# Optimization experiments

Hardware: AMD Instinct MI355X
Metric: run time of the kernel (lower is better)

Reference implementation:

```python
import jax, jax.numpy as jnp
import numpy as np

V, E, H, D, A, P = 8000, 384, 512, 512, 512, 128
B, N = 16, 128
NEG = -1.0e9


def _lstm(x, Wih, Whh, b, reverse=False):
    # x: (B, T, E); torch gate order i, f, g, o
    Hd = Whh.shape[1]
    def step(carry, xt):
        h, c = carry
        gates = xt @ Wih.T + h @ Whh.T + b
        i, f, g, o = jnp.split(gates, 4, axis=-1)
        c = jax.nn.sigmoid(f) * c + jax.nn.sigmoid(i) * jnp.tanh(g)
        h = jax.nn.sigmoid(o) * jnp.tanh(c)
        return (h, c), h
    xs = jnp.swapaxes(x, 0, 1)
    if reverse:
        xs = xs[::-1]
    init = (jnp.zeros((x.shape[0], Hd), x.dtype), jnp.zeros((x.shape[0], Hd), x.dtype))
    _, hs = jax.lax.scan(step, init, xs)
    if reverse:
        hs = hs[::-1]
    return jnp.swapaxes(hs, 0, 1)


def _forward(src_ids, src_mask, confusionset_mask, emb, Wih_f, Whh_f, b_f, Wih_b, Whh_b, b_b,
             Wih_d, Whh_d, b_d, W1, W2, v_att, combine_W, combine_b, vocab_W, vocab_b,
             Wg_W, Wg_b, ptr_W, ptr_b, ps_W, ps_b):
    x = emb[src_ids]                                                     # (B,N,E)
    # bidirectional encoder
    enc_hs = jnp.concatenate([_lstm(x, Wih_f, Whh_f, b_f),
                              _lstm(x, Wih_b, Whh_b, b_b, reverse=True)], axis=-1)  # (B,N,2H)
    # decoder LSTMCell unrolled over max_len=N steps (teacher forcing on src chars)
    dec_h = _lstm(x, Wih_d, Whh_d, b_d)                                  # (B,N,D)
    # Bahdanau additive attention
    dterm = dec_h @ W1.T                                                 # (B,N,A)
    eterm = enc_hs @ W2.T                                                # (B,N,A)
    score = jnp.tanh(dterm[:, :, None, :] + eterm[:, None, :, :]) @ v_att  # (B,T,n)
    score = jnp.where(src_mask[:, None, :] == 0, NEG, score)
    alpha = jax.nn.softmax(score, axis=-1)
    context = jnp.einsum('btn,bnh->bth', alpha, enc_hs)                  # (B,T,2H)
    combined = jnp.tanh(jnp.concatenate([dec_h, context], axis=-1) @ combine_W.T + combine_b)  # (B,T,D)
    vocab_logits = combined @ vocab_W.T + vocab_b                        # (B,T,V)
    vocab_logits = jnp.where(confusionset_mask == 0, NEG, vocab_logits)
    # pointer logits: Locj = (t == j) indicator as extra feature
    loc = jnp.eye(N, dtype=combined.dtype)                               # (T,n)
    base = combined @ ptr_W[:, :D].T + ptr_b                             # (B,T,P)
    ph = jnp.tanh(base[:, :, None, :] + loc[None, :, :, None] * ptr_W[:, D][None, None, None, :])  # (B,T,n,P)
    pos_scores = ph @ ps_W + ps_b                                        # (B,T,n)
    sentinel = jnp.tanh(combined @ Wg_W.T + Wg_b).sum(-1, keepdims=True) # (B,T,1)
    pointer_logits = jnp.concatenate([pos_scores, sentinel], axis=-1)    # (B,T,n+1)
    pad_mask = jnp.concatenate([src_mask, jnp.ones((src_mask.shape[0], 1), src_mask.dtype)], axis=1)
    pointer_logits = jnp.where(pad_mask[:, None, :] == 0, NEG, pointer_logits)
    return pointer_logits, vocab_logits


def setup_inputs():
    ks = iter(jax.random.split(jax.random.key(0), 40))
    def g(shape, s=0.05):
        return jax.random.normal(next(ks), shape, jnp.float32) * s
    inp = {
        'src_ids': jax.random.randint(next(ks), (B, N), 1, V),
        'src_mask': jnp.ones((B, N), jnp.int32),
        'confusionset_mask': jax.random.randint(next(ks), (B, N, V), 0, 2).astype(jnp.int32),
        'emb': g((V, E)).at[0].set(0.0),  # padding_idx=0 row zeroed
        'Wih_f': g((4 * H, E)), 'Whh_f': g((4 * H, H)), 'b_f': g((4 * H,)),
        'Wih_b': g((4 * H, E)), 'Whh_b': g((4 * H, H)), 'b_b': g((4 * H,)),
        'Wih_d': g((4 * D, E)), 'Whh_d': g((4 * D, D)), 'b_d': g((4 * D,)),
        'W1': g((A, D)), 'W2': g((A, 2 * H)), 'v_att': g((A,)),
        'combine_W': g((D, D + 2 * H)), 'combine_b': g((D,)),
        'vocab_W': g((V, D)), 'vocab_b': g((V,)),
        'Wg_W': g((D, D)), 'Wg_b': g((D,)),
        'ptr_W': g((P, D + 1)), 'ptr_b': g((P,)),
        'ps_W': g((P,)), 'ps_b': g(()),
    }
    return inp


def reference(src_ids, src_mask, confusionset_mask, emb, Wih_f, Whh_f, b_f, Wih_b, Whh_b, b_b,
              Wih_d, Whh_d, b_d, W1, W2, v_att, combine_W, combine_b, vocab_W, vocab_b,
              Wg_W, Wg_b, ptr_W, ptr_b, ps_W, ps_b):
    return _forward(src_ids, src_mask, confusionset_mask, emb, Wih_f, Whh_f, b_f, Wih_b, Whh_b, b_b,
                    Wih_d, Whh_d, b_d, W1, W2, v_att, combine_W, combine_b, vocab_W, vocab_b,
                    Wg_W, Wg_b, ptr_W, ptr_b, ps_W, ps_b)
```

## Files before the change

### kernel.cpp

```cpp
#include <hip/hip_runtime.h>
#include <hip/hip_bf16.h>
#include <math.h>

#define NEGV -1000000000.0f

static constexpr int B_ = 16, N_ = 128, BN_ = 2048;
static constexpr int E_ = 384, V_ = 8000;

typedef __attribute__((ext_vector_type(8))) short short8v;
typedef __attribute__((ext_vector_type(4))) float f32x4;

__device__ inline float wave_sum(float v) {
#pragma unroll
  for (int o = 32; o; o >>= 1) v += __shfl_xor(v, o);
  return v;
}
__device__ inline float wave_max(float v) {
#pragma unroll
  for (int o = 32; o; o >>= 1) v = fmaxf(v, __shfl_xor(v, o));
  return v;
}
__device__ inline float fast_tanh(float x) {
  return 1.f - 2.f / (1.f + __expf(2.f * x));
}
__device__ inline float fast_tanh_pre(float x2) {
  return 1.f - 2.f / (1.f + __expf(x2));
}
__device__ inline float fast_sig(float x) {
  return 1.f / (1.f + __expf(-x));
}
__device__ __forceinline__ void gl16(const void* g, void* l) {
  __builtin_amdgcn_global_load_lds((const __attribute__((address_space(1))) void*)g,
                                   (__attribute__((address_space(3))) void*)l, 16, 0, 0);
}

struct CastArgs {
  const float* s[6];
  unsigned long long d[6];
  int base[6];
  int total;
  int special;
};
__device__ inline void cast_body(const CastArgs& a, int gsize, int gid0) {
  const int nq = a.total >> 2;
  for (int q = gid0; q < nq; q += gsize) {
    const int e = q << 2;
    int k = 5;
    while (e < a.base[k]) --k;
    const int i = e - a.base[k];
    __hip_bfloat16* dst = (__hip_bfloat16*)a.d[k] + i;
    if (k == a.special) {
      const int row = i >> 9, col = i & 511;
      const float* sp = a.s[k] + (size_t)row * 513 + col;
#pragma unroll
      for (int u = 0; u < 4; ++u) dst[u] = __float2bfloat16(sp[u]);
    } else {
      float4 v = *(const float4*)(a.s[k] + i);
      __hip_bfloat16 h0 = __float2bfloat16(v.x), h1 = __float2bfloat16(v.y);
      __hip_bfloat16 h2 = __float2bfloat16(v.z), h3 = __float2bfloat16(v.w);
      ushort4 u4 = {*(unsigned short*)&h0, *(unsigned short*)&h1,
                    *(unsigned short*)&h2, *(unsigned short*)&h3};
      *(ushort4*)dst = u4;
    }
  }
}

__global__ __launch_bounds__(256) void prologue_kernel(
    const int* __restrict__ ids, const float* __restrict__ emb,
    __hip_bfloat16* __restrict__ xb, __hip_bfloat16* __restrict__ hbuf,
    CastArgs c1) {
  const int bid = blockIdx.x, tid = threadIdx.x;
  if (bid < 256) {
    for (int row = bid; row < 2048; row += 256) {
      const int id = ids[row];
      for (int e = tid; e < E_; e += 256)
        xb[(size_t)row * E_ + e] = __float2bfloat16(emb[(size_t)id * E_ + e]);
    }
  } else if (bid < 288) {
    const unsigned total = 3u * 128u * 8192u * 2u;
    const float pf = __builtin_bit_cast(float, 0x7f7f7f7fu);
    f32x4 pat = {pf, pf, pf, pf};
    char* base = (char*)hbuf;
    for (unsigned off = (unsigned)((bid - 256) * 256 + tid) * 16u; off < total;
         off += 32u * 256u * 16u) {
      asm volatile("global_store_dwordx4 %0, %1, %2 sc0 sc1"
                   :: "v"(off), "v"(pat), "s"(base) : "memory");
    }
  } else {
    cast_body(c1, 256 * 256, (bid - 288) * 256 + tid);
  }
}

template <int ACT, bool MASK>
__device__ __forceinline__ void gemm128_impl(
    const __hip_bfloat16* A, int lda, const __hip_bfloat16* W, int ldw,
    const float* bias, float* C, int ldc, __hip_bfloat16* Cb, int ldcb,
    int N, int K, const int* mask, int ldm, int m0, int n0,
    __hip_bfloat16 (*Al)[4096], __hip_bfloat16 (*Bl)[4096]) {
  const int tid = threadIdx.x;
  const int wid = tid >> 6, lane = tid & 63;
  const int nkt = K >> 5;
  const int rm = (wid >> 1) << 6, rn = (wid & 1) << 6;
  const int lrow = lane & 15, kq = lane >> 4;
  const int fs = ((lrow >> 1) & 3) << 4;

  f32x4 acc[4][4];
#pragma unroll
  for (int i = 0; i < 4; ++i)
#pragma unroll
    for (int j = 0; j < 4; ++j) acc[i][j] = {0.f, 0.f, 0.f, 0.f};

  auto stage = [&](int bi, int kt) {
#pragma unroll
    for (int c = 0; c < 2; ++c) {
      const int p = ((c * 4 + wid) << 6) + lane;
      const int row = p >> 2, cb = (p & 3) << 4;
      const int sw = ((row >> 1) & 3) << 4;
      const unsigned loff = (unsigned)__builtin_amdgcn_readfirstlane((c * 4 + wid) << 10);
      {
        const char* src = (const char*)A + ((size_t)(m0 + row) * lda + (size_t)kt * 32) * 2 + (cb ^ sw);
        gl16(src, (char*)&Al[bi][0] + loff);
      }
      {
        int gr = n0 + row;
        if (gr >= N) gr = N - 1;
        const char* src = (const char*)W + ((size_t)gr * ldw + (size_t)kt * 32) * 2 + (cb ^ sw);
        gl16(src, (char*)&Bl[bi][0] + loff);
      }
    }
  };
  auto compute = [&](int bi) {
    const char* Ab = (const char*)&Al[bi][0];
    const char* Bb = (const char*)&Bl[bi][0];
    const int roff = (kq << 4) ^ fs;
    short8v a[4], b[4];
#pragma unroll
    for (int i = 0; i < 4; ++i)
      a[i] = *(const short8v*)(Ab + (rm + i * 16 + lrow) * 64 + roff);
#pragma unroll
    for (int j = 0; j < 4; ++j)
      b[j] = *(const short8v*)(Bb + (rn + j * 16 + lrow) * 64 + roff);
#pragma unroll
    for (int i = 0; i < 4; ++i)
#pragma unroll
      for (int j = 0; j < 4; ++j)
        acc[i][j] = __builtin_amdgcn_mfma_f32_16x16x32_bf16(a[i], b[j], acc[i][j], 0, 0, 0);
  };

  stage(0, 0);
  for (int kt = 0; kt < nkt; ++kt) {
    __syncthreads();
    if (kt + 1 < nkt) stage((kt + 1) & 1, kt + 1);
    compute(kt & 1);
  }

#pragma unroll
  for (int i = 0; i < 4; ++i) {
#pragma unroll
    for (int r = 0; r < 4; ++r) {
      const int m = m0 + rm + i * 16 + kq * 4 + r;
#pragma unroll
      for (int j = 0; j < 4; ++j) {
        const int n = n0 + rn + j * 16 + lrow;
        if (n < N) {
          float v = acc[i][j][r] + (bias ? bias[n] : 0.f);
          if (ACT == 1) v = fast_tanh(v);
          if (MASK) {
            if (mask[(size_t)m * ldm + n] == 0) v = NEGV;
          }
          if (C) C[(size_t)m * ldc + n] = v;
          if (Cb) Cb[(size_t)m * ldcb + n] = __float2bfloat16(v);
        }
      }
    }
  }
}

__device__ __forceinline__ void gemm64_impl(
    const __hip_bfloat16* A, int lda, const __hip_bfloat16* W, int ldw,
    const float* bias, const float* bias2,
    float* C, int ldc, float* C2, __hip_bfloat16* Cb, int ldcb,
    int K, int act, int trout, int m0, int n0, char* AlB, char* BlB) {
  const int tid = threadIdx.x;
  const int wid = tid >> 6, lane = tid & 63;
  const int nkt = K >> 5;
  const int rm = (wid >> 1) << 5, rn = (wid & 1) << 5;
  const int lrow = lane & 15, kq = lane >> 4;
  const int fs = ((lrow >> 1) & 3) << 4;

  f32x4 acc[2][2];
#pragma unroll
  for (int i = 0; i < 2; ++i)
#pragma unroll
    for (int j = 0; j < 2; ++j) acc[i][j] = {0.f, 0.f, 0.f, 0.f};

  auto stage = [&](int bi, int kt) {
    const int row = tid >> 2, cb = (tid & 3) << 4;
    const int sw = ((row >> 1) & 3) << 4;
    const unsigned loff = (unsigned)__builtin_amdgcn_readfirstlane(wid << 10);
    {
      const char* src = (const char*)A + ((size_t)(m0 + row) * lda + (size_t)kt * 32) * 2 + (cb ^ sw);
      gl16(src, AlB + bi * 4096 + loff);
    }
    {
      const char* src = (const char*)W + ((size_t)(n0 + row) * ldw + (size_t)kt * 32) * 2 + (cb ^ sw);
      gl16(src, BlB + bi * 4096 + loff);
    }
  };
  auto compute = [&](int bi) {
    const char* Ab = AlB + bi * 4096;
    const char* Bb = BlB + bi * 4096;
    const int roff = (kq << 4) ^ fs;
    short8v a[2], b[2];
#pragma unroll
    for (int i = 0; i < 2; ++i)
      a[i] = *(const short8v*)(Ab + (rm + i * 16 + lrow) * 64 + roff);
#pragma unroll
    for (int j = 0; j < 2; ++j)
      b[j] = *(const short8v*)(Bb + (rn + j * 16 + lrow) * 64 + roff);
#pragma unroll
    for (int i = 0; i < 2; ++i)
#pragma unroll
      for (int j = 0; j < 2; ++j)
        acc[i][j] = __builtin_amdgcn_mfma_f32_16x16x32_bf16(a[i], b[j], acc[i][j], 0, 0, 0);
  };

  stage(0, 0);
  for (int kt = 0; kt < nkt; ++kt) {
    __syncthreads();
    if (kt + 1 < nkt) stage((kt + 1) & 1, kt + 1);
    compute(kt & 1);
  }

#pragma unroll
  for (int i = 0; i < 2; ++i) {
#pragma unroll
    for (int r = 0; r < 4; ++r) {
      const int m = m0 + rm + i * 16 + kq * 4 + r;
#pragma unroll
      for (int j = 0; j < 2; ++j) {
        const int n = n0 + rn + j * 16 + lrow;
        float v = acc[i][j][r];
        if (trout == 2) {
          if (n < 512) {
            C[(size_t)m * ldc + n] = fast_tanh(v + bias[n]);
          } else {
            C2[(size_t)m * 128 + (n - 512)] = v + bias2[n - 512];
          }
        } else {
          if (act == 2) v *= 2.f;
          else {
            v += (bias ? bias[n] : 0.f);
            if (act == 1) v = fast_tanh(v);
          }
          if (trout == 1) {
            Cb[(((size_t)(m >> 7) * 512 + n) << 7) + (m & 127)] = __float2bfloat16(v);
          } else {
            if (C) C[(size_t)m * ldc + n] = v;
            if (Cb) Cb[(size_t)m * ldcb + n] = __float2bfloat16(v);
          }
        }
      }
    }
  }
}

__global__ __launch_bounds__(256) void xproj_kernel(
    const __hip_bfloat16* __restrict__ A, const __hip_bfloat16* __restrict__ Wih,
    const float* __restrict__ b0, const float* __restrict__ b1,
    const float* __restrict__ b2, __hip_bfloat16* __restrict__ xproj16) {
  __shared__ __hip_bfloat16 Al[2][4096], Bl[2][4096];
  const int z = blockIdx.z;
  const float* bias = (z == 0) ? b0 : (z == 1 ? b1 : b2);
  gemm128_impl<0, false>(A, E_, Wih + (size_t)z * 2048 * 384, E_, bias,
                         nullptr, 0, xproj16 + (size_t)z * BN_ * 2048, 2048,
                         2048, E_, nullptr, 0, blockIdx.y * 128,
                         blockIdx.x * 128, Al, Bl);
}

__global__ __launch_bounds__(256) void qk_kernel(
    const __hip_bfloat16* __restrict__ catb, const __hip_bfloat16* __restrict__ ehsb,
    const __hip_bfloat16* __restrict__ w1, const __hip_bfloat16* __restrict__ w2,
    float* __restrict__ dterm, __hip_bfloat16* __restrict__ etT) {
  __shared__ char AlB[8192], BlB[8192];
  const int bid = blockIdx.x;
  if (bid < 256) {
    const int bx = bid & 7, by = bid >> 3;
    gemm64_impl(catb, 1536, w1, 512, nullptr, nullptr, dterm, 512, nullptr,
                nullptr, 0, 512, 2, 0, by * 64, bx * 64, AlB, BlB);
  } else {
    const int l = bid - 256;
    const int bx = l & 7, by = l >> 3;
    gemm64_impl(ehsb, 1024, w2, 1024, nullptr, nullptr, nullptr, 0, nullptr,
                etT, 0, 1024, 2, 1, by * 64, bx * 64, AlB, BlB);
  }
}

__global__ __launch_bounds__(256) void ctx_kernel(
    const __hip_bfloat16* __restrict__ alphab, const __hip_bfloat16* __restrict__ ehsT,
    __hip_bfloat16* __restrict__ catbCtx) {
  __shared__ char AlB[8192], BlB[8192];
  const int z = blockIdx.z;
  gemm64_impl(alphab + (size_t)z * 128 * 128, 128,
              ehsT + (size_t)z * 1024 * 128, 128, nullptr, nullptr, nullptr, 0,
              nullptr, catbCtx + (size_t)z * 128 * 1536, 1536, 128, 0, 0,
              blockIdx.y * 64, blockIdx.x * 64, AlB, BlB);
}

__global__ __launch_bounds__(256) void comb_kernel(
    const __hip_bfloat16* __restrict__ catb, const __hip_bfloat16* __restrict__ combw,
    const float* __restrict__ comb_b, __hip_bfloat16* __restrict__ combb) {
  __shared__ char AlB[8192], BlB[8192];
  gemm64_impl(catb, 1536, combw, 1536, comb_b, nullptr, nullptr, 0, nullptr,
              combb, 512, 1536, 1, 0, blockIdx.y * 64, blockIdx.x * 64, AlB, BlB);
}

__global__ __launch_bounds__(256) void tail_kernel(
    const __hip_bfloat16* __restrict__ combb, const __hip_bfloat16* __restrict__ vocw,
    const float* __restrict__ vocab_b, float* __restrict__ out1,
    const int* __restrict__ cmask,
    const __hip_bfloat16* __restrict__ wgw, const float* __restrict__ Wg_b,
    const float* __restrict__ ptr_b, float* __restrict__ wgout,
    float* __restrict__ baseb) {
  __shared__ __hip_bfloat16 Al[2][4096], Bl[2][4096];
  const int bid = blockIdx.x;
  if (bid < 1008) {
    const int bx = bid % 63, by = bid / 63;
    gemm128_impl<0, true>(combb, 512, vocw, 512, vocab_b, out1, V_, nullptr, 0,
                          V_, 512, cmask, V_, by * 128, bx * 128, Al, Bl);
  } else {
    const int l = bid - 1008;
    const int bx = l % 10, by = l / 10;
    gemm64_impl(combb, 512, wgw, 512, Wg_b, ptr_b, wgout, 512, baseb, nullptr,
                0, 512, 0, 2, by * 64, bx * 64, (char*)Al, (char*)Bl);
  }
}

__global__ __launch_bounds__(256) void fused_kernel(
    const __hip_bfloat16* __restrict__ xp16,
    const float* __restrict__ whhF, const float* __restrict__ whhB,
    const float* __restrict__ whhD,
    __hip_bfloat16* __restrict__ hbuf,
    __hip_bfloat16* __restrict__ ehsb, __hip_bfloat16* __restrict__ ehsT,
    __hip_bfloat16* __restrict__ catb,
    CastArgs ca2) {
  extern __shared__ char sm[];
  const int bid = blockIdx.x;
  const int tid = threadIdx.x;

  if (bid >= 96) {
    cast_body(ca2, 64 * 256, (bid - 96) * 256 + tid);
    return;
  }

  const int l = bid >> 5, g = bid & 31;
  const int lane = tid & 63, wid = tid >> 6;
  char* smW = sm;
  char* smH = sm + 65536;
  __hip_bfloat16* hout = (__hip_bfloat16*)(sm + 65536 + 16384);
  char* hist = sm + 65536 + 16384 + 512;

  const float* wsrc = (l == 0) ? whhF : ((l == 1) ? whhB : whhD);
  auto cv = [](float x) -> unsigned {
    __hip_bfloat16 h = __float2bfloat16(x);
    return (unsigned)*(unsigned short*)&h;
  };
  for (int p = tid; p < 4096; p += 256) {
    const int r = p >> 6, cb = (p & 63) << 4;
    const int grow = (r & 3) * 512 + (g << 4) + (r >> 2);
    const float* srcp = wsrc + (size_t)grow * 512 + ((p & 63) << 3);
    float4 u0 = *(const float4*)srcp;
    float4 u1 = *(const float4*)(srcp + 4);
    uint4 q;
    q.x = cv(u0.x) | (cv(u0.y) << 16);
    q.y = cv(u0.z) | (cv(u0.w) << 16);
    q.z = cv(u1.x) | (cv(u1.y) << 16);
    q.w = cv(u1.z) | (cv(u1.w) << 16);
    *(uint4*)(smW + r * 1024 + (cb ^ ((r & 7) << 4))) = q;
  }

  const int lrow = lane & 15, kq = lane >> 4;
  const int swz = (lrow & 7) << 4;
  const char* aB = smW + (wid * 16 + lrow) * 1024;
  const char* bB = smH + lrow * 1024;
  const int dl16 = wid * 4 + kq;
  const int dg = (g << 4) + dl16;
  const int bb = lrow;
  const bool rev = (l == 1);
  const __hip_bfloat16* xl = xp16 + (size_t)l * 2048 * 2048;
  __hip_bfloat16* hb_l = hbuf + (size_t)l * 128 * 8192;
  const int gq = tid >> 3;
  const int b0 = (tid & 7) * 2;
  const int gb = gq * 32;
  const int sw0 = (b0 & 7) << 4, sw1 = ((b0 + 1) & 7) << 4;
  float c = 0.f;

  for (int s = 0; s < 128; ++s) {
    const int t = rev ? 127 - s : s;
    const size_t xro = (size_t)(bb * 128 + t) * 2048 + dg;
    const float xgi = __bfloat162float(xl[xro]);
    const float xgf = __bfloat162float(xl[xro + 512]);
    const float xgg = __bfloat162float(xl[xro + 1024]);
    const float xgo = __bfloat162float(xl[xro + 1536]);

    if (s > 0) {
      if (gq != g) {
        const char* hsrc = (const char*)(hb_l + (size_t)(s - 1) * 8192);
        const unsigned loff = (unsigned)(tid * 64);
        unsigned hv;
        while (true) {
          asm volatile(
              "global_load_ushort %0, %1, %2 sc0 sc1\n\t"
              "s_waitcnt vmcnt(0)"
              : "=&v"(hv) : "v"(loff), "s"(hsrc) : "memory");
          if ((hv & 0xffffu) != 0x7f7fu) break;
          __builtin_amdgcn_s_sleep(1);
        }
        f32x4 q0, q1, q2, q3;
        asm volatile(
            "global_load_dwordx4 %0, %4, %5 sc0 sc1\n\t"
            "global_load_dwordx4 %1, %4, %5 offset:16 sc0 sc1\n\t"
            "global_load_dwordx4 %2, %4, %5 offset:32 sc0 sc1\n\t"
            "global_load_dwordx4 %3, %4, %5 offset:48 sc0 sc1\n\t"
            "s_waitcnt vmcnt(0)"
            : "=&v"(q0), "=&v"(q1), "=&v"(q2), "=&v"(q3)
            : "v"(loff), "s"(hsrc) : "memory");
        *(f32x4*)(smH + b0 * 1024 + (gb ^ sw0)) = q0;
        *(f32x4*)(smH + b0 * 1024 + ((gb + 16) ^ sw0)) = q1;
        *(f32x4*)(smH + (b0 + 1) * 1024 + (gb ^ sw1)) = q2;
        *(f32x4*)(smH + (b0 + 1) * 1024 + ((gb + 16) ^ sw1)) = q3;
      } else {
        const char* hl = (const char*)hout + b0 * 32;
        f32x4 c0 = *(const f32x4*)(hl);
        f32x4 c1 = *(const f32x4*)(hl + 16);
        f32x4 c2 = *(const f32x4*)(hl + 32);
        f32x4 c3 = *(const f32x4*)(hl + 48);
        *(f32x4*)(smH + b0 * 1024 + (gb ^ sw0)) = c0;
        *(f32x4*)(smH + b0 * 1024 + ((gb + 16) ^ sw0)) = c1;
        *(f32x4*)(smH + (b0 + 1) * 1024 + (gb ^ sw1)) = c2;
        *(f32x4*)(smH + (b0 + 1) * 1024 + ((gb + 16) ^ sw1)) = c3;
      }
    } else {
      const f32x4 z = {0.f, 0.f, 0.f, 0.f};
      *(f32x4*)(smH + b0 * 1024 + (gb ^ sw0)) = z;
      *(f32x4*)(smH + b0 * 1024 + ((gb + 16) ^ sw0)) = z;
      *(f32x4*)(smH + (b0 + 1) * 1024 + (gb ^ sw1)) = z;
      *(f32x4*)(smH + (b0 + 1) * 1024 + ((gb + 16) ^ sw1)) = z;
    }
    __syncthreads();

    f32x4 acc0 = {0.f, 0.f, 0.f, 0.f}, acc1 = {0.f, 0.f, 0.f, 0.f};
#pragma unroll
    for (int kt = 0; kt < 16; kt += 2) {
      const int off0 = ((kt * 64 + (kq << 4)) ^ swz);
      const int off1 = (((kt + 1) * 64 + (kq << 4)) ^ swz);
      short8v a0 = *(const short8v*)(aB + off0);
      short8v b0v = *(const short8v*)(bB + off0);
      short8v a1 = *(const short8v*)(aB + off1);
      short8v b1v = *(const short8v*)(bB + off1);
      acc0 = __builtin_amdgcn_mfma_f32_16x16x32_bf16(a0, b0v, acc0, 0, 0, 0);
      acc1 = __builtin_amdgcn_mfma_f32_16x16x32_bf16(a1, b1v, acc1, 0, 0, 0);
    }
    const f32x4 acc = acc0 + acc1;

    const float gi = acc[0] + xgi;
    const float gf = acc[1] + xgf;
    const float gg = acc[2] + xgg;
    const float go = acc[3] + xgo;
    c = fmaf(fast_sig(gf), c, fast_sig(gi) * fast_tanh(gg));
    const float h = fast_sig(go) * fast_tanh(c);
    __hip_bfloat16 hb16 = __float2bfloat16(h);
    const unsigned short hraw = *(unsigned short*)&hb16;
    hout[bb * 16 + dl16] = hb16;
    *(unsigned short*)(hist + s * 512 + (bb * 16 + dl16) * 2) = hraw;
    __syncthreads();

    if (s < 127 && wid == (s & 3) && (lane < 32)) {
      f32x4 hv4 = *(const f32x4*)((const char*)hout + lane * 16);
      char* hdst = (char*)(hb_l + (size_t)s * 8192);
      asm volatile("global_store_dwordx4 %0, %1, %2 sc0 sc1"
                   :: "v"((unsigned)((g << 9) + lane * 16)), "v"(hv4), "s"(hdst)
                   : "memory");
    }
  }

  __syncthreads();
  const int bb2 = tid >> 4, lo2 = tid & 15;
  if (l < 2) {
    const int hoff = (bb2 * 16 + lo2) * 2;
    char* dstT = (char*)(ehsT + ((size_t)bb2 * 1024 + l * 512 + (g << 4) + lo2) * 128);
    for (int tc = 0; tc < 128; tc += 32) {
      unsigned v[16];
#pragma unroll
      for (int w = 0; w < 16; ++w) {
        const int t0 = tc + 2 * w;
        const int s0 = rev ? 127 - t0 : t0;
        const int s1 = rev ? 126 - t0 : t0 + 1;
        unsigned a = *(const unsigned short*)(hist + s0 * 512 + hoff);
        unsigned b2 = *(const unsigned short*)(hist + s1 * 512 + hoff);
        v[w] = a | (b2 << 16);
      }
#pragma unroll
      for (int q = 0; q < 4; ++q)
        *(uint4*)(dstT + tc * 2 + q * 16) =
            make_uint4(v[q * 4], v[q * 4 + 1], v[q * 4 + 2], v[q * 4 + 3]);
    }
    for (int k = 0; k < 8; ++k) {
      const int t = lo2 * 8 + k;
      const int s0 = rev ? 127 - t : t;
      const char* srcp = hist + s0 * 512 + bb2 * 32;
      uint4 ra = *(const uint4*)srcp;
      uint4 rb = *(const uint4*)(srcp + 16);
      char* dp = (char*)(ehsb + ((size_t)(bb2 * 128 + t)) * 1024 + l * 512 + (g << 4));
      *(uint4*)dp = ra;
      *(uint4*)(dp + 16) = rb;
    }
  } else {
    for (int k = 0; k < 8; ++k) {
      const int t = lo2 * 8 + k;
      const char* srcp = hist + t * 512 + bb2 * 32;
      uint4 ra = *(const uint4*)srcp;
      uint4 rb = *(const uint4*)(srcp + 16);
      char* dp = (char*)(catb + ((size_t)(bb2 * 128 + t)) * 1536 + (g << 4));
      *(uint4*)dp = ra;
      *(uint4*)(dp + 16) = rb;
    }
  }
}

__global__ __launch_bounds__(256) void score_kernel(
    const float* __restrict__ dterm, const __hip_bfloat16* __restrict__ etT,
    const float* __restrict__ v_att, const int* __restrict__ src_mask,
    __hip_bfloat16* __restrict__ alphab) {
  const int b = blockIdx.x >> 5, tg = blockIdx.x & 31;
  const int t0 = tg * 4;
  const int tid = threadIdx.x;
  __shared__ float dt[4][512], vs[512], red[4][4][128], al[4][128];
  for (int i = tid; i < 2048; i += 256)
    dt[i >> 9][i & 511] = dterm[((size_t)(b * 128 + t0 + (i >> 9))) * 512 + (i & 511)];
  vs[tid] = v_att[tid];
  vs[tid + 256] = v_att[256 + tid];
  __syncthreads();
  const int n0 = (tid & 63) << 1, ah = tid >> 6;
  {
    const __hip_bfloat16* ep = etT + (((size_t)b * 512 + ah * 128) << 7) + n0;
    const float* vp = vs + ah * 128;
    const float* dp0 = &dt[0][ah * 128];
    const float* dp1 = &dt[1][ah * 128];
    const float* dp2 = &dt[2][ah * 128];
    const float* dp3 = &dt[3][ah * 128];
    float p00 = 0, p01 = 0, p10 = 0, p11 = 0, p20 = 0, p21 = 0, p30 = 0, p31 = 0;
    for (int a = 0; a < 128; ++a) {
      const unsigned u = *(const unsigned*)(ep + ((size_t)a << 7));
      unsigned u0 = u << 16, u1 = u & 0xffff0000u;
      const float e0 = __builtin_bit_cast(float, u0);
      const float e1 = __builtin_bit_cast(float, u1);
      const float va = vp[a];
      p00 = fmaf(va, fast_tanh_pre(dp0[a] + e0), p00);
      p01 = fmaf(va, fast_tanh_pre(dp0[a] + e1), p01);
      p10 = fmaf(va, fast_tanh_pre(dp1[a] + e0), p10);
      p11 = fmaf(va, fast_tanh_pre(dp1[a] + e1), p11);
      p20 = fmaf(va, fast_tanh_pre(dp2[a] + e0), p20);
      p21 = fmaf(va, fast_tanh_pre(dp2[a] + e1), p21);
      p30 = fmaf(va, fast_tanh_pre(dp3[a] + e0), p30);
      p31 = fmaf(va, fast_tanh_pre(dp3[a] + e1), p31);
    }
    red[0][ah][n0] = p00; red[0][ah][n0 + 1] = p01;
    red[1][ah][n0] = p10; red[1][ah][n0 + 1] = p11;
    red[2][ah][n0] = p20; red[2][ah][n0 + 1] = p21;
    red[3][ah][n0] = p30; red[3][ah][n0 + 1] = p31;
  }
  __syncthreads();
#pragma unroll
  for (int tp = 0; tp < 2; ++tp) {
    const int tt = tp * 2 + (tid >> 7);
    const int n = tid & 127;
    float sc = red[tt][0][n] + red[tt][1][n] + red[tt][2][n] + red[tt][3][n];
    if (src_mask[b * 128 + n] == 0) sc = NEGV;
    al[tt][n] = sc;
  }
  __syncthreads();
  {
    const int tt = tid >> 6, lane = tid & 63;
    const float v0 = al[tt][lane], v1 = al[tt][lane + 64];
    const float m = wave_max(fmaxf(v0, v1));
    const float e0 = __expf(v0 - m), e1 = __expf(v1 - m);
    const float inv = 1.f / wave_sum(e0 + e1);
    __hip_bfloat16* ap = alphab + ((size_t)(b * 128 + t0 + tt)) * 128;
    ap[lane] = __float2bfloat16(e0 * inv);
    ap[lane + 64] = __float2bfloat16(e1 * inv);
  }
}

__global__ __launch_bounds__(256) void pointer_kernel(
    const float* __restrict__ base, const float* __restrict__ wgout,
    const float* __restrict__ ptr_W, const float* __restrict__ ps_W,
    const float* __restrict__ ps_b, const int* __restrict__ src_mask,
    float* __restrict__ out0) {
  const int bt = blockIdx.x;
  const int b = bt >> 7, t = bt & 127;
  const int tid = threadIdx.x;
  __shared__ float r0[4], r1[4], r2[4], fin[3];
  float off_p = 0.f, diag_p = 0.f, sent_p;
  if (tid < 128) {
    const float ba = base[(size_t)bt * 128 + tid];
    const float pw = ps_W[tid];
    off_p = tanhf(ba) * pw;
    diag_p = tanhf(ba + ptr_W[tid * 513 + 512]) * pw;
  }
  sent_p = wgout[(size_t)bt * 512 + tid] + wgout[(size_t)bt * 512 + 256 + tid];
  off_p = wave_sum(off_p);
  diag_p = wave_sum(diag_p);
  sent_p = wave_sum(sent_p);
  const int wid = tid >> 6, lane = tid & 63;
  if (lane == 0) { r0[wid] = off_p; r1[wid] = diag_p; r2[wid] = sent_p; }
  __syncthreads();
  if (tid == 0) {
    const float psb = ps_b[0];
    fin[0] = r0[0] + r0[1] + r0[2] + r0[3] + psb;
    fin[1] = r1[0] + r1[1] + r1[2] + r1[3] + psb;
    fin[2] = r2[0] + r2[1] + r2[2] + r2[3];
  }
  __syncthreads();
  const float s_off = fin[0], s_diag = fin[1], sent = fin[2];
  if (tid < 129) {
    float v;
    if (tid == 128) v = sent;
    else {
      v = (tid == t) ? s_diag : s_off;
      if (src_mask[b * 128 + tid] == 0) v = NEGV;
    }
    out0[(size_t)bt * 129 + tid] = v;
  }
}

extern "C" void kernel_launch(void* const* d_in, const int* in_sizes, int n_in,
                              void* d_out, int out_size, void* d_ws, size_t ws_size,
                              hipStream_t stream) {
  const int* src_ids   = (const int*)d_in[0];
  const int* src_mask  = (const int*)d_in[1];
  const int* cmask     = (const int*)d_in[2];
  const float* emb     = (const float*)d_in[3];
  const float* Wih_f   = (const float*)d_in[4];
  const float* Whh_f   = (const float*)d_in[5];
  const float* b_f     = (const float*)d_in[6];
  const float* Wih_b   = (const float*)d_in[7];
  const float* Whh_b   = (const float*)d_in[8];
  const float* b_b     = (const float*)d_in[9];
  const float* Wih_d   = (const float*)d_in[10];
  const float* Whh_d   = (const float*)d_in[11];
  const float* b_d     = (const float*)d_in[12];
  const float* W1      = (const float*)d_in[13];
  const float* W2      = (const float*)d_in[14];
  const float* v_att   = (const float*)d_in[15];
  const float* comb_W  = (const float*)d_in[16];
  const float* comb_b  = (const float*)d_in[17];
  const float* vocab_W = (const float*)d_in[18];
  const float* vocab_b = (const float*)d_in[19];
  const float* Wg_W    = (const float*)d_in[20];
  const float* Wg_b    = (const float*)d_in[21];
  const float* ptr_W   = (const float*)d_in[22];
  const float* ptr_b   = (const float*)d_in[23];
  const float* ps_W    = (const float*)d_in[24];
  const float* ps_b    = (const float*)d_in[25];
  (void)in_sizes; (void)n_in; (void)out_size; (void)ws_size;

  char* wsb = (char*)d_ws;
  size_t o = 0;
  auto alloc = [&](size_t bytes) { char* p = wsb + o; o = (o + bytes + 255) & ~(size_t)255; return p; };
  __hip_bfloat16* xb      = (__hip_bfloat16*)alloc((size_t)BN_ * E_ * 2);
  __hip_bfloat16* xproj16 = (__hip_bfloat16*)alloc((size_t)3 * BN_ * 2048 * 2);
  __hip_bfloat16* ehsb    = (__hip_bfloat16*)alloc((size_t)BN_ * 1024 * 2);
  __hip_bfloat16* ehsT    = (__hip_bfloat16*)alloc((size_t)16 * 1024 * 128 * 2);
  __hip_bfloat16* catb    = (__hip_bfloat16*)alloc((size_t)BN_ * 1536 * 2);
  float* dterm            = (float*)alloc((size_t)BN_ * 512 * 4);
  __hip_bfloat16* etT     = (__hip_bfloat16*)alloc((size_t)16 * 512 * 128 * 2);
  __hip_bfloat16* alphab  = (__hip_bfloat16*)alloc((size_t)BN_ * 128 * 2);
  __hip_bfloat16* combb   = (__hip_bfloat16*)alloc((size_t)BN_ * 512 * 2);
  float* wgout            = (float*)alloc((size_t)BN_ * 512 * 4);
  float* baseb            = (float*)alloc((size_t)BN_ * 128 * 4);
  __hip_bfloat16* hbuf    = (__hip_bfloat16*)alloc((size_t)3 * 128 * 8192 * 2);
  __hip_bfloat16* wih16   = (__hip_bfloat16*)alloc((size_t)3 * 2048 * 384 * 2);
  __hip_bfloat16* w1_16   = (__hip_bfloat16*)alloc((size_t)512 * 512 * 2);
  __hip_bfloat16* w2_16   = (__hip_bfloat16*)alloc((size_t)512 * 1024 * 2);
  __hip_bfloat16* combw16 = (__hip_bfloat16*)alloc((size_t)512 * 1536 * 2);
  __hip_bfloat16* vocw16  = (__hip_bfloat16*)alloc((size_t)8000 * 512 * 2);
  __hip_bfloat16* wgw16   = (__hip_bfloat16*)alloc((size_t)512 * 512 * 2);
  __hip_bfloat16* ptrw16  = (__hip_bfloat16*)alloc((size_t)128 * 512 * 2);

  float* out0 = (float*)d_out;
  float* out1 = out0 + (size_t)BN_ * 129;

  CastArgs c1;
  {
    const float* s3[3] = {Wih_f, Wih_b, Wih_d};
    int acc = 0;
    for (int k = 0; k < 3; ++k) {
      c1.s[k] = s3[k];
      c1.d[k] = (unsigned long long)(wih16 + (size_t)k * 2048 * 384);
      c1.base[k] = acc;
      acc += 2048 * 384;
    }
    for (int k = 3; k < 6; ++k) { c1.s[k] = nullptr; c1.d[k] = 0; c1.base[k] = 0x7fffffff; }
    c1.total = acc; c1.special = -1;
  }
  CastArgs c2;
  {
    const float* s6[6] = {W1, W2, comb_W, vocab_W, Wg_W, ptr_W};
    __hip_bfloat16* d6[6] = {w1_16, w2_16, combw16, vocw16, wgw16, ptrw16};
    int ns[6] = {512 * 512, 512 * 1024, 512 * 1536, 8000 * 512, 512 * 512, 128 * 512};
    int acc = 0;
    for (int k = 0; k < 6; ++k) {
      c2.s[k] = s6[k]; c2.d[k] = (unsigned long long)d6[k]; c2.base[k] = acc;
      acc += ns[k];
    }
    c2.total = acc; c2.special = 5;
  }

  prologue_kernel<<<544, 256, 0, stream>>>(src_ids, emb, xb, hbuf, c1);

  xproj_kernel<<<dim3(16, 16, 3), 256, 0, stream>>>(
      xb, wih16, b_f, b_b, b_d, xproj16);

  hipError_t e1 = hipFuncSetAttribute((const void*)fused_kernel,
                      hipFuncAttributeMaxDynamicSharedMemorySize, 147968);
  (void)e1;
  fused_kernel<<<160, 256, 147968, stream>>>(
      xproj16, Whh_f, Whh_b, Whh_d, hbuf, ehsb, ehsT, catb, c2);

  qk_kernel<<<512, 256, 0, stream>>>(catb, ehsb, w1_16, w2_16, dterm, etT);

  score_kernel<<<16 * 32, 256, 0, stream>>>(dterm, etT, v_att, src_mask, alphab);

  ctx_kernel<<<dim3(16, 2, 16), 256, 0, stream>>>(alphab, ehsT, catb + 512);

  comb_kernel<<<dim3(8, 32), 256, 0, stream>>>(catb, combw16, comb_b, combb);

  tail_kernel<<<1328, 256, 0, stream>>>(combb, vocw16, vocab_b, out1, cmask,
                                        wgw16, Wg_b, ptr_b, wgout, baseb);

  pointer_kernel<<<BN_, 256, 0, stream>>>(baseb, wgout, ptr_W, ps_W, ps_b, src_mask, out0);
}
```

Measured before the change: 586.6 us.

## Merge post-LSTM attention stages into one cooperative kernel and retile xproj layout

Replaces the separate qk, score, ctx, comb, Wg and pointer kernel launches with a single cooperative kernel of 512 blocks that uses grid-wide syncs between stages, with the vocab GEMM left as its own kernel at the end. The goal is to remove launch gaps and tail effects between the small dependent stages. Separately, the xproj GEMM now writes its output in a layout indexed by timestep, so the recurrent loop reads each step's gate inputs from a contiguous region. In exchange, the cooperative launch requires all 512 blocks to be co-resident, and each grid sync leaves blocks idle in stages where only some of them have work.

```diff
diff --git a/kernel.cpp b/kernel.cpp
--- a/kernel.cpp
+++ b/kernel.cpp
@@ -1,6 +1,9 @@
 #include <hip/hip_runtime.h>
 #include <hip/hip_bf16.h>
+#include <hip/hip_cooperative_groups.h>
 #include <math.h>
+
+namespace cg = cooperative_groups;
 
 #define NEGV -1000000000.0f
 
@@ -91,12 +94,12 @@
   }
 }
 
-template <int ACT, bool MASK>
+template <int ACT, int MASK, int OUT>
 __device__ __forceinline__ void gemm128_impl(
     const __hip_bfloat16* A, int lda, const __hip_bfloat16* W, int ldw,
     const float* bias, float* C, int ldc, __hip_bfloat16* Cb, int ldcb,
-    int N, int K, const int* mask, int ldm, int m0, int n0,
-    __hip_bfloat16 (*Al)[4096], __hip_bfloat16 (*Bl)[4096]) {
+    int N, int K, const int* maskp, int ldm, int m0, int n0,
+    char* smA, char* smB) {
   const int tid = threadIdx.x;
   const int wid = tid >> 6, lane = tid & 63;
   const int nkt = K >> 5;
@@ -119,19 +122,19 @@
       const unsigned loff = (unsigned)__builtin_amdgcn_readfirstlane((c * 4 + wid) << 10);
       {
         const char* src = (const char*)A + ((size_t)(m0 + row) * lda + (size_t)kt * 32) * 2 + (cb ^ sw);
-        gl16(src, (char*)&Al[bi][0] + loff);
+        gl16(src, smA + bi * 8192 + loff);
       }
       {
         int gr = n0 + row;
         if (gr >= N) gr = N - 1;
         const char* src = (const char*)W + ((size_t)gr * ldw + (size_t)kt * 32) * 2 + (cb ^ sw);
-        gl16(src, (char*)&Bl[bi][0] + loff);
+        gl16(src, smB + bi * 8192 + loff);
       }
     }
   };
   auto compute = [&](int bi) {
-    const char* Ab = (const char*)&Al[bi][0];
-    const char* Bb = (const char*)&Bl[bi][0];
+    const char* Ab = smA + bi * 8192;
+    const char* Bb = smB + bi * 8192;
     const int roff = (kq << 4) ^ fs;
     short8v a[4], b[4];
 #pragma unroll
@@ -165,11 +168,17 @@
         if (n < N) {
           float v = acc[i][j][r] + (bias ? bias[n] : 0.f);
           if (ACT == 1) v = fast_tanh(v);
-          if (MASK) {
-            if (mask[(size_t)m * ldm + n] == 0) v = NEGV;
+          if (MASK == 1) {
+            if (maskp[(size_t)m * ldm + n] == 0) v = NEGV;
           }
-          if (C) C[(size_t)m * ldc + n] = v;
-          if (Cb) Cb[(size_t)m * ldcb + n] = __float2bfloat16(v);
+          if (OUT == 3) {
+            const size_t idx = (((size_t)(m & 127) * 32 + ((n >> 4) & 31)) * 4 +
+                               (n >> 9)) * 256 + (((size_t)(m >> 7)) << 4) + (n & 15);
+            Cb[idx] = __float2bfloat16(v);
+          } else {
+            if (C) C[(size_t)m * ldc + n] = v;
+            if (Cb) Cb[(size_t)m * ldcb + n] = __float2bfloat16(v);
+          }
         }
       }
     }
@@ -268,76 +277,29 @@
 __global__ __launch_bounds__(256) void xproj_kernel(
     const __hip_bfloat16* __restrict__ A, const __hip_bfloat16* __restrict__ Wih,
     const float* __restrict__ b0, const float* __restrict__ b1,
-    const float* __restrict__ b2, __hip_bfloat16* __restrict__ xproj16) {
-  __shared__ __hip_bfloat16 Al[2][4096], Bl[2][4096];
+    const float* __restrict__ b2, __hip_bfloat16* __restrict__ xpT) {
+  __shared__ __align__(16) char smA[16384], smB[16384];
   const int z = blockIdx.z;
   const float* bias = (z == 0) ? b0 : (z == 1 ? b1 : b2);
-  gemm128_impl<0, false>(A, E_, Wih + (size_t)z * 2048 * 384, E_, bias,
-                         nullptr, 0, xproj16 + (size_t)z * BN_ * 2048, 2048,
-                         2048, E_, nullptr, 0, blockIdx.y * 128,
-                         blockIdx.x * 128, Al, Bl);
-}
-
-__global__ __launch_bounds__(256) void qk_kernel(
-    const __hip_bfloat16* __restrict__ catb, const __hip_bfloat16* __restrict__ ehsb,
-    const __hip_bfloat16* __restrict__ w1, const __hip_bfloat16* __restrict__ w2,
-    float* __restrict__ dterm, __hip_bfloat16* __restrict__ etT) {
-  __shared__ char AlB[8192], BlB[8192];
-  const int bid = blockIdx.x;
-  if (bid < 256) {
-    const int bx = bid & 7, by = bid >> 3;
-    gemm64_impl(catb, 1536, w1, 512, nullptr, nullptr, dterm, 512, nullptr,
-                nullptr, 0, 512, 2, 0, by * 64, bx * 64, AlB, BlB);
-  } else {
-    const int l = bid - 256;
-    const int bx = l & 7, by = l >> 3;
-    gemm64_impl(ehsb, 1024, w2, 1024, nullptr, nullptr, nullptr, 0, nullptr,
-                etT, 0, 1024, 2, 1, by * 64, bx * 64, AlB, BlB);
-  }
-}
-
-__global__ __launch_bounds__(256) void ctx_kernel(
-    const __hip_bfloat16* __restrict__ alphab, const __hip_bfloat16* __restrict__ ehsT,
-    __hip_bfloat16* __restrict__ catbCtx) {
-  __shared__ char AlB[8192], BlB[8192];
-  const int z = blockIdx.z;
-  gemm64_impl(alphab + (size_t)z * 128 * 128, 128,
-              ehsT + (size_t)z * 1024 * 128, 128, nullptr, nullptr, nullptr, 0,
-              nullptr, catbCtx + (size_t)z * 128 * 1536, 1536, 128, 0, 0,
-              blockIdx.y * 64, blockIdx.x * 64, AlB, BlB);
-}
-
-__global__ __launch_bounds__(256) void comb_kernel(
-    const __hip_bfloat16* __restrict__ catb, const __hip_bfloat16* __restrict__ combw,
-    const float* __restrict__ comb_b, __hip_bfloat16* __restrict__ combb) {
-  __shared__ char AlB[8192], BlB[8192];
-  gemm64_impl(catb, 1536, combw, 1536, comb_b, nullptr, nullptr, 0, nullptr,
-              combb, 512, 1536, 1, 0, blockIdx.y * 64, blockIdx.x * 64, AlB, BlB);
-}
-
-__global__ __launch_bounds__(256) void tail_kernel(
+  gemm128_impl<0, 0, 3>(A, E_, Wih + (size_t)z * 2048 * 384, E_, bias,
+                        nullptr, 0, xpT + (size_t)z * 2048 * 2048, 0,
+                        2048, E_, nullptr, 0, blockIdx.y * 128,
+                        blockIdx.x * 128, smA, smB);
+}
+
+__global__ __launch_bounds__(256) void vocab_kernel(
     const __hip_bfloat16* __restrict__ combb, const __hip_bfloat16* __restrict__ vocw,
     const float* __restrict__ vocab_b, float* __restrict__ out1,
-    const int* __restrict__ cmask,
-    const __hip_bfloat16* __restrict__ wgw, const float* __restrict__ Wg_b,
-    const float* __restrict__ ptr_b, float* __restrict__ wgout,
-    float* __restrict__ baseb) {
-  __shared__ __hip_bfloat16 Al[2][4096], Bl[2][4096];
+    const int* __restrict__ cmask) {
+  __shared__ __align__(16) char smA[16384], smB[16384];
   const int bid = blockIdx.x;
-  if (bid < 1008) {
-    const int bx = bid % 63, by = bid / 63;
-    gemm128_impl<0, true>(combb, 512, vocw, 512, vocab_b, out1, V_, nullptr, 0,
-                          V_, 512, cmask, V_, by * 128, bx * 128, Al, Bl);
-  } else {
-    const int l = bid - 1008;
-    const int bx = l % 10, by = l / 10;
-    gemm64_impl(combb, 512, wgw, 512, Wg_b, ptr_b, wgout, 512, baseb, nullptr,
-                0, 512, 0, 2, by * 64, bx * 64, (char*)Al, (char*)Bl);
-  }
+  const int bx = bid % 63, by = bid / 63;
+  gemm128_impl<0, 1, 0>(combb, 512, vocw, 512, vocab_b, out1, V_, nullptr, 0,
+                        V_, 512, cmask, V_, by * 128, bx * 128, smA, smB);
 }
 
 __global__ __launch_bounds__(256) void fused_kernel(
-    const __hip_bfloat16* __restrict__ xp16,
+    const __hip_bfloat16* __restrict__ xpT,
     const float* __restrict__ whhF, const float* __restrict__ whhB,
     const float* __restrict__ whhD,
     __hip_bfloat16* __restrict__ hbuf,
@@ -387,7 +349,7 @@
   const int dg = (g << 4) + dl16;
   const int bb = lrow;
   const bool rev = (l == 1);
-  const __hip_bfloat16* xl = xp16 + (size_t)l * 2048 * 2048;
+  const __hip_bfloat16* xl = xpT + (size_t)l * 2048 * 2048;
   __hip_bfloat16* hb_l = hbuf + (size_t)l * 128 * 8192;
   const int gq = tid >> 3;
   const int b0 = (tid & 7) * 2;
@@ -397,11 +359,11 @@
 
   for (int s = 0; s < 128; ++s) {
     const int t = rev ? 127 - s : s;
-    const size_t xro = (size_t)(bb * 128 + t) * 2048 + dg;
-    const float xgi = __bfloat162float(xl[xro]);
-    const float xgf = __bfloat162float(xl[xro + 512]);
-    const float xgg = __bfloat162float(xl[xro + 1024]);
-    const float xgo = __bfloat162float(xl[xro + 1536]);
+    const __hip_bfloat16* xt = xl + (size_t)t * 32768 + (g << 10) + (bb << 4) + dl16;
+    const float xgi = __bfloat162float(xt[0]);
+    const float xgf = __bfloat162float(xt[256]);
+    const float xgg = __bfloat162float(xt[512]);
+    const float xgo = __bfloat162float(xt[768]);
 
     if (s > 0) {
       if (gq != g) {
@@ -528,42 +490,49 @@
   }
 }
 
-__global__ __launch_bounds__(256) void score_kernel(
-    const float* __restrict__ dterm, const __hip_bfloat16* __restrict__ etT,
-    const float* __restrict__ v_att, const int* __restrict__ src_mask,
-    __hip_bfloat16* __restrict__ alphab) {
-  const int b = blockIdx.x >> 5, tg = blockIdx.x & 31;
+struct CoopArgs {
+  const __hip_bfloat16 *catb, *ehsb, *w1, *w2, *ehsT, *combw, *wgw;
+  __hip_bfloat16 *catbw, *etT, *alphab, *combb;
+  const float *v_att, *comb_b, *Wg_b, *ptr_b, *ptr_W, *ps_W, *ps_b;
+  const int* src_mask;
+  float *dterm, *wgout, *baseb, *out0;
+};
+
+__device__ void score_body(const CoopArgs& a, int bid, int tid, char* smbuf) {
+  const int b = bid >> 5, tg = bid & 31;
   const int t0 = tg * 4;
-  const int tid = threadIdx.x;
-  __shared__ float dt[4][512], vs[512], red[4][4][128], al[4][128];
+  float (*dt)[512] = (float(*)[512])smbuf;
+  float* vs = (float*)(smbuf + 8192);
+  float (*red)[4][128] = (float(*)[4][128])(smbuf + 10240);
+  float (*al)[128] = (float(*)[128])(smbuf + 18432);
   for (int i = tid; i < 2048; i += 256)
-    dt[i >> 9][i & 511] = dterm[((size_t)(b * 128 + t0 + (i >> 9))) * 512 + (i & 511)];
-  vs[tid] = v_att[tid];
-  vs[tid + 256] = v_att[256 + tid];
+    dt[i >> 9][i & 511] = a.dterm[((size_t)(b * 128 + t0 + (i >> 9))) * 512 + (i & 511)];
+  vs[tid] = a.v_att[tid];
+  vs[tid + 256] = a.v_att[256 + tid];
   __syncthreads();
   const int n0 = (tid & 63) << 1, ah = tid >> 6;
   {
-    const __hip_bfloat16* ep = etT + (((size_t)b * 512 + ah * 128) << 7) + n0;
+    const __hip_bfloat16* ep = a.etT + (((size_t)b * 512 + ah * 128) << 7) + n0;
     const float* vp = vs + ah * 128;
     const float* dp0 = &dt[0][ah * 128];
     const float* dp1 = &dt[1][ah * 128];
     const float* dp2 = &dt[2][ah * 128];
     const float* dp3 = &dt[3][ah * 128];
     float p00 = 0, p01 = 0, p10 = 0, p11 = 0, p20 = 0, p21 = 0, p30 = 0, p31 = 0;
-    for (int a = 0; a < 128; ++a) {
-      const unsigned u = *(const unsigned*)(ep + ((size_t)a << 7));
+    for (int q = 0; q < 128; ++q) {
+      const unsigned u = *(const unsigned*)(ep + ((size_t)q << 7));
       unsigned u0 = u << 16, u1 = u & 0xffff0000u;
       const float e0 = __builtin_bit_cast(float, u0);
       const float e1 = __builtin_bit_cast(float, u1);
-      const float va = vp[a];
-      p00 = fmaf(va, fast_tanh_pre(dp0[a] + e0), p00);
-      p01 = fmaf(va, fast_tanh_pre(dp0[a] + e1), p01);
-      p10 = fmaf(va, fast_tanh_pre(dp1[a] + e0), p10);
-      p11 = fmaf(va, fast_tanh_pre(dp1[a] + e1), p11);
-      p20 = fmaf(va, fast_tanh_pre(dp2[a] + e0), p20);
-      p21 = fmaf(va, fast_tanh_pre(dp2[a] + e1), p21);
-      p30 = fmaf(va, fast_tanh_pre(dp3[a] + e0), p30);
-      p31 = fmaf(va, fast_tanh_pre(dp3[a] + e1), p31);
+      const float va = vp[q];
+      p00 = fmaf(va, fast_tanh_pre(dp0[q] + e0), p00);
+      p01 = fmaf(va, fast_tanh_pre(dp0[q] + e1), p01);
+      p10 = fmaf(va, fast_tanh_pre(dp1[q] + e0), p10);
+      p11 = fmaf(va, fast_tanh_pre(dp1[q] + e1), p11);
+      p20 = fmaf(va, fast_tanh_pre(dp2[q] + e0), p20);
+      p21 = fmaf(va, fast_tanh_pre(dp2[q] + e1), p21);
+      p30 = fmaf(va, fast_tanh_pre(dp3[q] + e0), p30);
+      p31 = fmaf(va, fast_tanh_pre(dp3[q] + e1), p31);
     }
     red[0][ah][n0] = p00; red[0][ah][n0 + 1] = p01;
     red[1][ah][n0] = p10; red[1][ah][n0 + 1] = p11;
@@ -576,7 +545,7 @@
     const int tt = tp * 2 + (tid >> 7);
     const int n = tid & 127;
     float sc = red[tt][0][n] + red[tt][1][n] + red[tt][2][n] + red[tt][3][n];
-    if (src_mask[b * 128 + n] == 0) sc = NEGV;
+    if (a.src_mask[b * 128 + n] == 0) sc = NEGV;
     al[tt][n] = sc;
   }
   __syncthreads();
@@ -586,29 +555,26 @@
     const float m = wave_max(fmaxf(v0, v1));
     const float e0 = __expf(v0 - m), e1 = __expf(v1 - m);
     const float inv = 1.f / wave_sum(e0 + e1);
-    __hip_bfloat16* ap = alphab + ((size_t)(b * 128 + t0 + tt)) * 128;
+    __hip_bfloat16* ap = a.alphab + ((size_t)(b * 128 + t0 + tt)) * 128;
     ap[lane] = __float2bfloat16(e0 * inv);
     ap[lane + 64] = __float2bfloat16(e1 * inv);
   }
 }
 
-__global__ __launch_bounds__(256) void pointer_kernel(
-    const float* __restrict__ base, const float* __restrict__ wgout,
-    const float* __restrict__ ptr_W, const float* __restrict__ ps_W,
-    const float* __restrict__ ps_b, const int* __restrict__ src_mask,
-    float* __restrict__ out0) {
-  const int bt = blockIdx.x;
+__device__ void pointer_body(const CoopArgs& a, int bt, int tid, char* smbuf) {
   const int b = bt >> 7, t = bt & 127;
-  const int tid = threadIdx.x;
-  __shared__ float r0[4], r1[4], r2[4], fin[3];
+  float* r0 = (float*)smbuf;
+  float* r1 = r0 + 4;
+  float* r2 = r0 + 8;
+  float* fin = r0 + 12;
   float off_p = 0.f, diag_p = 0.f, sent_p;
   if (tid < 128) {
-    const float ba = base[(size_t)bt * 128 + tid];
-    const float pw = ps_W[tid];
+    const float ba = a.baseb[(size_t)bt * 128 + tid];
+    const float pw = a.ps_W[tid];
     off_p = tanhf(ba) * pw;
-    diag_p = tanhf(ba + ptr_W[tid * 513 + 512]) * pw;
-  }
-  sent_p = wgout[(size_t)bt * 512 + tid] + wgout[(size_t)bt * 512 + 256 + tid];
+    diag_p = tanhf(ba + a.ptr_W[tid * 513 + 512]) * pw;
+  }
+  sent_p = a.wgout[(size_t)bt * 512 + tid] + a.wgout[(size_t)bt * 512 + 256 + tid];
   off_p = wave_sum(off_p);
   diag_p = wave_sum(diag_p);
   sent_p = wave_sum(sent_p);
@@ -616,7 +582,7 @@
   if (lane == 0) { r0[wid] = off_p; r1[wid] = diag_p; r2[wid] = sent_p; }
   __syncthreads();
   if (tid == 0) {
-    const float psb = ps_b[0];
+    const float psb = a.ps_b[0];
     fin[0] = r0[0] + r0[1] + r0[2] + r0[3] + psb;
     fin[1] = r1[0] + r1[1] + r1[2] + r1[3] + psb;
     fin[2] = r2[0] + r2[1] + r2[2] + r2[3];
@@ -628,10 +594,58 @@
     if (tid == 128) v = sent;
     else {
       v = (tid == t) ? s_diag : s_off;
-      if (src_mask[b * 128 + tid] == 0) v = NEGV;
-    }
-    out0[(size_t)bt * 129 + tid] = v;
-  }
+      if (a.src_mask[b * 128 + tid] == 0) v = NEGV;
+    }
+    a.out0[(size_t)bt * 129 + tid] = v;
+  }
+  __syncthreads();
+}
+
+__global__ __launch_bounds__(256) void coop_kernel(CoopArgs a) {
+  __shared__ __align__(16) char smbuf[40960];
+  cg::grid_group grid = cg::this_grid();
+  const int bid = blockIdx.x, tid = threadIdx.x;
+
+  if (bid < 256) {
+    gemm64_impl(a.catb, 1536, a.w1, 512, nullptr, nullptr, a.dterm, 512,
+                nullptr, nullptr, 0, 512, 2, 0, (bid >> 3) * 64, (bid & 7) * 64,
+                smbuf, smbuf + 8192);
+  } else {
+    const int l = bid - 256;
+    gemm64_impl(a.ehsb, 1024, a.w2, 1024, nullptr, nullptr, nullptr, 0,
+                nullptr, a.etT, 0, 1024, 2, 1, (l >> 3) * 64, (l & 7) * 64,
+                smbuf, smbuf + 8192);
+  }
+  grid.sync();
+
+  score_body(a, bid, tid, smbuf);
+  grid.sync();
+
+  {
+    const int z = bid >> 5, r = bid & 31;
+    gemm64_impl(a.alphab + (size_t)z * 128 * 128, 128,
+                a.ehsT + (size_t)z * 1024 * 128, 128, nullptr, nullptr,
+                nullptr, 0, nullptr, a.catbw + 512 + (size_t)z * 128 * 1536,
+                1536, 128, 0, 0, (r >> 4) * 64, (r & 15) * 64,
+                smbuf, smbuf + 8192);
+  }
+  grid.sync();
+
+  if (bid < 256) {
+    gemm64_impl(a.catb, 1536, a.combw, 1536, a.comb_b, nullptr, nullptr, 0,
+                nullptr, a.combb, 512, 1536, 1, 0, (bid >> 3) * 64,
+                (bid & 7) * 64, smbuf, smbuf + 8192);
+  }
+  grid.sync();
+
+  if (bid < 320) {
+    gemm64_impl(a.combb, 512, a.wgw, 512, a.Wg_b, a.ptr_b, a.wgout, 512,
+                a.baseb, nullptr, 0, 512, 0, 2, (bid / 10) * 64,
+                (bid % 10) * 64, smbuf, smbuf + 8192);
+  }
+  grid.sync();
+
+  for (int bt = bid; bt < 2048; bt += 512) pointer_body(a, bt, tid, smbuf);
 }
 
 extern "C" void kernel_launch(void* const* d_in, const int* in_sizes, int n_in,
@@ -669,7 +683,7 @@
   size_t o = 0;
   auto alloc = [&](size_t bytes) { char* p = wsb + o; o = (o + bytes + 255) & ~(size_t)255; return p; };
   __hip_bfloat16* xb      = (__hip_bfloat16*)alloc((size_t)BN_ * E_ * 2);
-  __hip_bfloat16* xproj16 = (__hip_bfloat16*)alloc((size_t)3 * BN_ * 2048 * 2);
+  __hip_bfloat16* xpT     = (__hip_bfloat16*)alloc((size_t)3 * BN_ * 2048 * 2);
   __hip_bfloat16* ehsb    = (__hip_bfloat16*)alloc((size_t)BN_ * 1024 * 2);
   __hip_bfloat16* ehsT    = (__hip_bfloat16*)alloc((size_t)16 * 1024 * 128 * 2);
   __hip_bfloat16* catb    = (__hip_bfloat16*)alloc((size_t)BN_ * 1536 * 2);
@@ -719,25 +733,26 @@
 
   prologue_kernel<<<544, 256, 0, stream>>>(src_ids, emb, xb, hbuf, c1);
 
-  xproj_kernel<<<dim3(16, 16, 3), 256, 0, stream>>>(
-      xb, wih16, b_f, b_b, b_d, xproj16);
+  xproj_kernel<<<dim3(16, 16, 3), 256, 0, stream>>>(xb, wih16, b_f, b_b, b_d, xpT);
 
   hipError_t e1 = hipFuncSetAttribute((const void*)fused_kernel,
                       hipFuncAttributeMaxDynamicSharedMemorySize, 147968);
   (void)e1;
   fused_kernel<<<160, 256, 147968, stream>>>(
-      xproj16, Whh_f, Whh_b, Whh_d, hbuf, ehsb, ehsT, catb, c2);
-
-  qk_kernel<<<512, 256, 0, stream>>>(catb, ehsb, w1_16, w2_16, dterm, etT);
-
-  score_kernel<<<16 * 32, 256, 0, stream>>>(dterm, etT, v_att, src_mask, alphab);
-
-  ctx_kernel<<<dim3(16, 2, 16), 256, 0, stream>>>(alphab, ehsT, catb + 512);
-
-  comb_kernel<<<dim3(8, 32), 256, 0, stream>>>(catb, combw16, comb_b, combb);
-
-  tail_kernel<<<1328, 256, 0, stream>>>(combb, vocw16, vocab_b, out1, cmask,
-                                        wgw16, Wg_b, ptr_b, wgout, baseb);
-
-  pointer_kernel<<<BN_, 256, 0, stream>>>(baseb, wgout, ptr_W, ps_W, ps_b, src_mask, out0);
-}
+      xpT, Whh_f, Whh_b, Whh_d, hbuf, ehsb, ehsT, catb, c2);
+
+  CoopArgs ca;
+  ca.catb = catb; ca.ehsb = ehsb; ca.w1 = w1_16; ca.w2 = w2_16; ca.ehsT = ehsT;
+  ca.combw = combw16; ca.wgw = wgw16;
+  ca.catbw = catb; ca.etT = etT; ca.alphab = alphab; ca.combb = combb;
+  ca.v_att = v_att; ca.comb_b = comb_b; ca.Wg_b = Wg_b;
+  ca.ptr_b = ptr_b; ca.ptr_W = ptr_W; ca.ps_W = ps_W; ca.ps_b = ps_b;
+  ca.src_mask = src_mask;
+  ca.dterm = dterm; ca.wgout = wgout; ca.baseb = baseb; ca.out0 = out0;
+  void* kargs[] = {&ca};
+  hipError_t e2 = hipLaunchCooperativeKernel((const void*)coop_kernel,
+                                             dim3(512), dim3(256), kargs, 0, stream);
+  (void)e2;
+
+  vocab_kernel<<<1008, 256, 0, stream>>>(combb, vocw16, vocab_b, out1, cmask);
+}
```

Result: slower. 903.0 us (+53.9%).
